# Performance work log

Hardware: AMD Instinct MI355X
Metric: run time of the kernel (lower is better)

Reference implementation:

```python
import jax, jax.numpy as jnp
import numpy as np

NUM_HEADS = 8
NUM_POINTS = 4


def _bilinear_sample(value_hw, locs, H, W):
    """grid_sample(mode='bilinear', align_corners=False, padding_mode='zeros').
    value_hw: [B, heads, H*W, hd]; locs: [B, Nq, heads, P, 2] in [0,1].
    Returns [B, Nq, heads, P, hd]."""
    B, Nq, heads, P, _ = locs.shape
    hd = value_hw.shape[-1]
    # torch maps g in [-1,1] -> pixel ((g+1)*size-1)/2; with g = 2*loc-1 this is loc*size - 0.5
    x = locs[..., 0] * W - 0.5
    y = locs[..., 1] * H - 0.5
    x0 = jnp.floor(x); y0 = jnp.floor(y)
    wx = x - x0; wy = y - y0
    ix0 = x0.astype(jnp.int32); iy0 = y0.astype(jnp.int32)
    ix1 = ix0 + 1; iy1 = iy0 + 1

    def gather(iy, ix):
        valid = (ix >= 0) & (ix < W) & (iy >= 0) & (iy < H)
        flat = jnp.clip(iy, 0, H - 1) * W + jnp.clip(ix, 0, W - 1)  # [B,Nq,heads,P]
        flat_t = flat.transpose(0, 2, 1, 3).reshape(B, heads, Nq * P)
        v = jnp.take_along_axis(value_hw, flat_t[..., None], axis=2)  # [B,heads,Nq*P,hd]
        v = v.reshape(B, heads, Nq, P, hd).transpose(0, 2, 1, 3, 4)
        return v * valid[..., None].astype(v.dtype)

    out = (gather(iy0, ix0) * ((1 - wx) * (1 - wy))[..., None]
           + gather(iy0, ix1) * (wx * (1 - wy))[..., None]
           + gather(iy1, ix0) * ((1 - wx) * wy)[..., None]
           + gather(iy1, ix1) * (wx * wy)[..., None])
    return out


def setup_inputs() -> dict:
    key = jax.random.key(0)
    ks = jax.random.split(key, 12)
    B, Nq, C, H, W = 4, 8192, 256, 128, 128
    heads, P = NUM_HEADS, NUM_POINTS
    s = 1.0 / np.sqrt(C)
    return {
        "query": jax.random.normal(ks[0], (B, Nq, C), jnp.float32),
        "reference_points": jax.random.uniform(ks[1], (B, Nq, 2), jnp.float32),
        "value": jax.random.normal(ks[2], (B, H * W, C), jnp.float32),
        "W_off": jax.random.normal(ks[3], (C, heads * P * 2), jnp.float32) * s,
        "b_off": jax.random.normal(ks[4], (heads * P * 2,), jnp.float32) * 0.5,
        "W_attn": jax.random.normal(ks[5], (C, heads * P), jnp.float32) * s,
        "b_attn": jax.random.normal(ks[6], (heads * P,), jnp.float32) * 0.1,
        "W_v": jax.random.normal(ks[7], (C, C), jnp.float32) * s,
        "b_v": jax.random.normal(ks[8], (C,), jnp.float32) * 0.1,
        "W_out": jax.random.normal(ks[9], (C, C), jnp.float32) * s,
        "b_out": jax.random.normal(ks[10], (C,), jnp.float32) * 0.1,
        "H": H,
        "W": W,
    }


def reference(query, reference_points, value, W_off, b_off, W_attn, b_attn,
              W_v, b_v, W_out, b_out, H, W):
    B, Nq, C = query.shape
    heads, P = NUM_HEADS, NUM_POINTS
    hd = C // heads

    offsets = (query @ W_off + b_off).reshape(B, Nq, heads, P, 2)
    attn = jax.nn.softmax((query @ W_attn + b_attn).reshape(B, Nq, heads, P), axis=-1)

    off_x = offsets[..., 0] / float(W) * 0.1
    off_y = offsets[..., 1] / float(H) * 0.1
    locs = reference_points[:, :, None, None, :] + jnp.stack([off_x, off_y], axis=-1)
    locs = jnp.clip(locs, 0.0, 1.0)  # [B,Nq,heads,P,2]

    # value projection -> [B, heads, H*W, hd]
    v = (value @ W_v + b_v).reshape(B, H * W, heads, hd).transpose(0, 2, 1, 3)

    sampled = _bilinear_sample(v, locs, H, W)            # [B,Nq,heads,P,hd]
    agg = jnp.einsum('bnhp,bnhpd->bnhd', attn, sampled)  # weighted sum over points
    out = agg.reshape(B, Nq, C) @ W_out + b_out
    return out
```

## Files before the change

kernel.cpp:

```cpp
#include <hip/hip_runtime.h>
#include <cstdint>

#define NB 4
#define NQ 8192
#define NC 256
#define IH 128
#define IW 128
#define NHW (IH * IW)
#define NHEADS 8
#define NP 4
#define NHD 32

typedef __bf16 bf16x8 __attribute__((ext_vector_type(8)));
typedef float f32x4 __attribute__((ext_vector_type(4)));

union FragCast { uint4 q; bf16x8 v; };

__device__ __forceinline__ unsigned int f2bf(float f) {
    unsigned int u = __float_as_uint(f);
    return (u + 0x7FFFu + ((u >> 16) & 1u)) >> 16;
}
__device__ __forceinline__ float bf2f(unsigned short s) {
    return __uint_as_float(((unsigned int)s) << 16);
}

__global__ __launch_bounds__(256) void k_pack(
    const float* __restrict__ Wv, const float* __restrict__ Wout,
    const float* __restrict__ Woff, const float* __restrict__ Wattn,
    unsigned short* __restrict__ pkv, unsigned short* __restrict__ pko,
    unsigned short* __restrict__ pkq)
{
    const int tid = blockIdx.x * 256 + threadIdx.x;
    if (tid < 4096) {
        const float* src = (tid & 2048) ? Wout : Wv;
        unsigned short* dst = (tid & 2048) ? pko : pkv;
        const int rem = tid & 2047;
        const int kt = rem >> 8, col = rem & 255;
        unsigned short* d = dst + (size_t)kt * 8192 + (col >> 4) * 512 + (col & 15) * 8;
        const float* s = src + (size_t)kt * 32 * 256 + col;
#pragma unroll
        for (int j = 0; j < 32; ++j)
            d[(j >> 3) * 128 + (j & 7)] = (unsigned short)f2bf(s[(size_t)j * 256]);
    } else {
        const int rem = tid - 4096;
        const int kt = rem / 96, col = rem % 96;
        unsigned short* d = pkq + (size_t)kt * 3072 + (col >> 4) * 512 + (col & 15) * 8;
        const float* s; int stride;
        if (col < 64) { s = Woff + col; stride = 64; }
        else          { s = Wattn + (col - 64); stride = 32; }
        s += (size_t)kt * 32 * stride;
#pragma unroll
        for (int j = 0; j < 32; ++j)
            d[(j >> 3) * 128 + (j & 7)] = (unsigned short)f2bf(s[(size_t)j * stride]);
    }
}

#define VP_TPB 4
__global__ __launch_bounds__(512) void k_vproj(
    const float* __restrict__ value, const unsigned short* __restrict__ Bpk,
    const float* __restrict__ bv, unsigned short* __restrict__ vproj)
{
    const int t = threadIdx.x;
    const int l = t & 63, w = t >> 6;
    const int mh = w & 1, cg = w >> 1;

    __shared__ unsigned short A[2][64 * 256];

    uint4 bq[8][4];
#pragma unroll
    for (int kt = 0; kt < 8; ++kt)
#pragma unroll
        for (int i = 0; i < 4; ++i)
            bq[kt][i] = *reinterpret_cast<const uint4*>(
                Bpk + (size_t)kt * 8192 + (size_t)(cg * 4 + i) * 512 + l * 8);

    float bb[4];
#pragma unroll
    for (int i = 0; i < 4; ++i) bb[i] = bv[cg * 64 + i * 16 + (l & 15)];

    const size_t tile0 = (size_t)blockIdx.x * VP_TPB;

    float4 st[8];
#pragma unroll
    for (int i = 0; i < 8; ++i) {
        const int chunk = i * 512 + t;
        const int row = chunk >> 6, k0 = (chunk & 63) * 4;
        st[i] = *reinterpret_cast<const float4*>(&value[(tile0 * 64 + row) * NC + k0]);
    }
#pragma unroll
    for (int i = 0; i < 8; ++i) {
        const int chunk = i * 512 + t;
        const int row = chunk >> 6, k0 = (chunk & 63) * 4;
        unsigned int byte = (unsigned int)(row * 512 + k0 * 2) ^ (unsigned int)((row & 7) << 4);
        *reinterpret_cast<uint2*>(reinterpret_cast<char*>(A[0]) + byte) =
            make_uint2(f2bf(st[i].x) | (f2bf(st[i].y) << 16),
                       f2bf(st[i].z) | (f2bf(st[i].w) << 16));
    }
    __syncthreads();

    for (int tt = 0; tt < VP_TPB; ++tt) {
        const int cur = tt & 1;
        if (tt + 1 < VP_TPB) {
#pragma unroll
            for (int i = 0; i < 8; ++i) {
                const int chunk = i * 512 + t;
                const int row = chunk >> 6, k0 = (chunk & 63) * 4;
                st[i] = *reinterpret_cast<const float4*>(
                    &value[((tile0 + tt + 1) * 64 + row) * NC + k0]);
            }
        }

        f32x4 acc[2][4];
#pragma unroll
        for (int m = 0; m < 2; ++m)
#pragma unroll
            for (int i = 0; i < 4; ++i) acc[m][i] = (f32x4)(bb[i]);

#pragma unroll
        for (int kt = 0; kt < 8; ++kt) {
#pragma unroll
            for (int m = 0; m < 2; ++m) {
                const int arow = mh * 32 + m * 16 + (l & 15);
                unsigned int abyte = (unsigned int)(arow * 512 + (kt * 32 + (l >> 4) * 8) * 2)
                                   ^ (unsigned int)((arow & 7) << 4);
                FragCast af;
                af.q = *reinterpret_cast<const uint4*>(reinterpret_cast<const char*>(A[cur]) + abyte);
#pragma unroll
                for (int i = 0; i < 4; ++i) {
                    FragCast bfc; bfc.q = bq[kt][i];
                    acc[m][i] = __builtin_amdgcn_mfma_f32_16x16x32_bf16(af.v, bfc.v, acc[m][i], 0, 0, 0);
                }
            }
        }

        const size_t rowbase = (tile0 + tt) * 64;
#pragma unroll
        for (int m = 0; m < 2; ++m)
#pragma unroll
            for (int i = 0; i < 4; ++i) {
                const int col = cg * 64 + i * 16 + (l & 15);
#pragma unroll
                for (int j = 0; j < 4; ++j) {
                    const size_t row = rowbase + mh * 32 + m * 16 + (l >> 4) * 4 + j;
                    vproj[row * NC + col] = (unsigned short)f2bf(acc[m][i][j]);
                }
            }

        if (tt + 1 < VP_TPB) {
#pragma unroll
            for (int i = 0; i < 8; ++i) {
                const int chunk = i * 512 + t;
                const int row = chunk >> 6, k0 = (chunk & 63) * 4;
                unsigned int byte = (unsigned int)(row * 512 + k0 * 2) ^ (unsigned int)((row & 7) << 4);
                *reinterpret_cast<uint2*>(reinterpret_cast<char*>(A[cur ^ 1]) + byte) =
                    make_uint2(f2bf(st[i].x) | (f2bf(st[i].y) << 16),
                               f2bf(st[i].z) | (f2bf(st[i].w) << 16));
            }
            __syncthreads();
        }
    }
}

__global__ __launch_bounds__(512) void k_fused(
    const float* __restrict__ query, const float* __restrict__ refp,
    const unsigned short* __restrict__ Bq, const float* __restrict__ boff,
    const float* __restrict__ battn, const unsigned short* __restrict__ vproj,
    const unsigned short* __restrict__ Bo, const float* __restrict__ bout,
    float* __restrict__ out)
{
    const int t = threadIdx.x;
    const int l = t & 63, w = t >> 6;
    const int x = blockIdx.x & 7, kk = blockIdx.x >> 3;
    const int b = x >> 1;
    const int j = (kk << 1) | (x & 1);
    const size_t q0 = (size_t)b * NQ + (size_t)j * 16;

    __shared__ unsigned short A[16 * 256];
    __shared__ float locs_s[16][64];
    __shared__ float attn_s[16][32];
    __shared__ float refs[16][2];

#pragma unroll
    for (int i = 0; i < 2; ++i) {
        const int chunk = i * 512 + t;
        const int row = chunk >> 6, k0 = (chunk & 63) * 4;
        const float4 v4 = *reinterpret_cast<const float4*>(&query[(q0 + row) * NC + k0]);
        unsigned int byte = (unsigned int)(row * 512 + k0 * 2) ^ (unsigned int)((row & 7) << 4);
        *reinterpret_cast<uint2*>(reinterpret_cast<char*>(A) + byte) =
            make_uint2(f2bf(v4.x) | (f2bf(v4.y) << 16),
                       f2bf(v4.z) | (f2bf(v4.w) << 16));
    }
    if (t < 32) reinterpret_cast<float*>(refs)[t] = refp[q0 * 2 + t];
    __syncthreads();

    if (w < 6) {
        const int arow = l & 15, achunk = l >> 4;
        f32x4 acc = (f32x4)(0.f);
#pragma unroll
        for (int kt = 0; kt < 8; ++kt) {
            unsigned int abyte = (unsigned int)(arow * 512 + (kt * 32 + achunk * 8) * 2)
                               ^ (unsigned int)((arow & 7) << 4);
            FragCast af;
            af.q = *reinterpret_cast<const uint4*>(reinterpret_cast<const char*>(A) + abyte);
            FragCast bfc;
            bfc.q = *reinterpret_cast<const uint4*>(Bq + (size_t)kt * 3072 + w * 512 + l * 8);
            acc = __builtin_amdgcn_mfma_f32_16x16x32_bf16(af.v, bfc.v, acc, 0, 0, 0);
        }
        const int col = w * 16 + arow;
        if (col < 64) {
            const float bias = boff[col];
            const int xy = col & 1;
#pragma unroll
            for (int jj = 0; jj < 4; ++jj) {
                const int row = achunk * 4 + jj;
                float off = acc[jj] + bias;
                float loc = refs[row][xy] + off * (0.1f / 128.0f);
                locs_s[row][col] = fminf(fmaxf(loc, 0.f), 1.f);
            }
        } else {
            const int lc = col - 64;
            const float bias = battn[lc];
#pragma unroll
            for (int jj = 0; jj < 4; ++jj) {
                const int row = achunk * 4 + jj;
                float v = acc[jj] + bias;
                float m = fmaxf(v, __shfl_xor(v, 1));
                m = fmaxf(m, __shfl_xor(m, 2));
                float e = __expf(v - m);
                float s = e + __shfl_xor(e, 1);
                s = s + __shfl_xor(s, 2);
                attn_s[row][lc] = e / s;
            }
        }
    }
    __syncthreads();

    {
        const int q = t >> 5, h = (t >> 2) & 7, c = t & 3;
        const char* __restrict__ vb =
            reinterpret_cast<const char*>(vproj) + (size_t)b * NHW * 512;
        const unsigned int laneoff = (unsigned int)(h * 64 + c * 16);

        float wts[16];
        unsigned int offs[16];
#pragma unroll
        for (int p = 0; p < 4; ++p) {
            const float lx = locs_s[q][h * 8 + p * 2 + 0];
            const float ly = locs_s[q][h * 8 + p * 2 + 1];
            const float aw = attn_s[q][h * 4 + p];
            const float xx = lx * (float)IW - 0.5f;
            const float yy = ly * (float)IH - 0.5f;
            const float x0f = floorf(xx), y0f = floorf(yy);
            const float wx = xx - x0f, wy = yy - y0f;
            const int ix0 = (int)x0f, iy0 = (int)y0f;
            const int ix1 = ix0 + 1, iy1 = iy0 + 1;
            const int cx0 = max(ix0, 0), cy0 = max(iy0, 0);
            const int cx1 = min(ix1, IW - 1), cy1 = min(iy1, IH - 1);
            const float vx0 = (ix0 >= 0) ? 1.f : 0.f;
            const float vy0 = (iy0 >= 0) ? 1.f : 0.f;
            const float vx1 = (ix1 < IW) ? 1.f : 0.f;
            const float vy1 = (iy1 < IH) ? 1.f : 0.f;
            wts[p * 4 + 0] = aw * ((1.f - wx) * (1.f - wy) * vx0 * vy0);
            wts[p * 4 + 1] = aw * (wx * (1.f - wy) * vx1 * vy0);
            wts[p * 4 + 2] = aw * ((1.f - wx) * wy * vx0 * vy1);
            wts[p * 4 + 3] = aw * (wx * wy * vx1 * vy1);
            offs[p * 4 + 0] = (unsigned int)(cy0 * IW + cx0) * 512u + laneoff;
            offs[p * 4 + 1] = (unsigned int)(cy0 * IW + cx1) * 512u + laneoff;
            offs[p * 4 + 2] = (unsigned int)(cy1 * IW + cx0) * 512u + laneoff;
            offs[p * 4 + 3] = (unsigned int)(cy1 * IW + cx1) * 512u + laneoff;
        }

        uint4 vals[16];
#pragma unroll
        for (int jj = 0; jj < 16; ++jj)
            vals[jj] = *reinterpret_cast<const uint4*>(vb + offs[jj]);

        float acc[8];
#pragma unroll
        for (int e = 0; e < 8; ++e) acc[e] = 0.f;
#pragma unroll
        for (int jj = 0; jj < 16; ++jj) {
            const unsigned short* u = reinterpret_cast<const unsigned short*>(&vals[jj]);
            const float wj = wts[jj];
#pragma unroll
            for (int e = 0; e < 8; ++e) acc[e] = fmaf(wj, bf2f(u[e]), acc[e]);
        }

        uint4 pk;
        pk.x = f2bf(acc[0]) | (f2bf(acc[1]) << 16);
        pk.y = f2bf(acc[2]) | (f2bf(acc[3]) << 16);
        pk.z = f2bf(acc[4]) | (f2bf(acc[5]) << 16);
        pk.w = f2bf(acc[6]) | (f2bf(acc[7]) << 16);
        unsigned int byte = (unsigned int)(q * 512 + (h * NHD + c * 8) * 2)
                          ^ (unsigned int)((q & 7) << 4);
        *reinterpret_cast<uint4*>(reinterpret_cast<char*>(A) + byte) = pk;
    }
    __syncthreads();

    {
        const int arow = l & 15, achunk = l >> 4;
        f32x4 acc2[2];
#pragma unroll
        for (int i = 0; i < 2; ++i) acc2[i] = (f32x4)(0.f);

#pragma unroll
        for (int kt = 0; kt < 8; ++kt) {
            unsigned int abyte = (unsigned int)(arow * 512 + (kt * 32 + achunk * 8) * 2)
                               ^ (unsigned int)((arow & 7) << 4);
            FragCast af;
            af.q = *reinterpret_cast<const uint4*>(reinterpret_cast<const char*>(A) + abyte);
#pragma unroll
            for (int i = 0; i < 2; ++i) {
                const int ct = w * 2 + i;
                FragCast bfc;
                bfc.q = *reinterpret_cast<const uint4*>(Bo + (size_t)kt * 8192 + ct * 512 + l * 8);
                acc2[i] = __builtin_amdgcn_mfma_f32_16x16x32_bf16(af.v, bfc.v, acc2[i], 0, 0, 0);
            }
        }

#pragma unroll
        for (int i = 0; i < 2; ++i) {
            const int col = (w * 2 + i) * 16 + arow;
            const float bbv = bout[col];
#pragma unroll
            for (int jj = 0; jj < 4; ++jj) {
                const size_t row = q0 + achunk * 4 + jj;
                out[row * NC + col] = acc2[i][jj] + bbv;
            }
        }
    }
}

extern "C" void kernel_launch(void* const* d_in, const int* in_sizes, int n_in,
                              void* d_out, int out_size, void* d_ws, size_t ws_size,
                              hipStream_t stream) {
    const float* query = (const float*)d_in[0];
    const float* refp  = (const float*)d_in[1];
    const float* value = (const float*)d_in[2];
    const float* Woff  = (const float*)d_in[3];
    const float* boff  = (const float*)d_in[4];
    const float* Wattn = (const float*)d_in[5];
    const float* battn = (const float*)d_in[6];
    const float* Wv    = (const float*)d_in[7];
    const float* bv    = (const float*)d_in[8];
    const float* Wout  = (const float*)d_in[9];
    const float* bout  = (const float*)d_in[10];
    float* out = (float*)d_out;

    unsigned short* vproj  = (unsigned short*)d_ws;
    unsigned short* WvPk   = vproj + (size_t)NB * NHW * NC;
    unsigned short* WoutPk = WvPk + (size_t)NC * NC;
    unsigned short* WqPk   = WoutPk + (size_t)NC * NC;

    k_pack<<<dim3(19), dim3(256), 0, stream>>>(Wv, Wout, Woff, Wattn, WvPk, WoutPk, WqPk);
    k_vproj<<<dim3(256), dim3(512), 0, stream>>>(value, WvPk, bv, vproj);
    k_fused<<<dim3(NB * NQ / 16), dim3(512), 0, stream>>>(query, refp, WqPk, boff, battn,
                                                          vproj, WoutPk, bout, out);
}
```

Baseline: 67.33 us.

## Sort queries by spatial bin of reference point for gather locality

Adds a counting sort (count, scan, scatter kernels) that groups queries into 16x16 spatial bins by reference point, then has the fused kernel process queries in that order using an indirection array. The goal is to make each block's bilinear gathers from the projected value tensor hit nearby pixels, which improves cache reuse. In exchange it adds four small launches, including a memset and a single-thread serial scan, and replaces contiguous query loads and output stores with indirect row accesses. Atomic-based slot assignment makes the order within a bin nondeterministic, but the output is unaffected.

Result: slower. 83.56 us (+24.1%).

```diff
diff --git a/kernel.cpp b/kernel.cpp
--- a/kernel.cpp
+++ b/kernel.cpp
@@ -22,6 +22,43 @@
 }
 __device__ __forceinline__ float bf2f(unsigned short s) {
     return __uint_as_float(((unsigned int)s) << 16);
+}
+__device__ __forceinline__ int ref_bin(float rx, float ry) {
+    int bx = (int)(rx * 16.0f); bx = bx > 15 ? 15 : (bx < 0 ? 0 : bx);
+    int by = (int)(ry * 16.0f); by = by > 15 ? 15 : (by < 0 ? 0 : by);
+    return by * 16 + bx;
+}
+
+__global__ __launch_bounds__(256) void k_count(
+    const float* __restrict__ refp, int* __restrict__ cnt)
+{
+    const int tid = blockIdx.x * 256 + threadIdx.x;
+    const int b = tid >> 13;
+    const int bin = ref_bin(refp[(size_t)tid * 2], refp[(size_t)tid * 2 + 1]);
+    atomicAdd(&cnt[b * 256 + bin], 1);
+}
+
+__global__ __launch_bounds__(64) void k_scan(
+    const int* __restrict__ cnt, int* __restrict__ pos)
+{
+    const int b = threadIdx.x;
+    if (b < NB) {
+        int run = b * NQ;
+        for (int i = 0; i < 256; ++i) {
+            pos[b * 256 + i] = run;
+            run += cnt[b * 256 + i];
+        }
+    }
+}
+
+__global__ __launch_bounds__(256) void k_scatter(
+    const float* __restrict__ refp, int* __restrict__ pos, int* __restrict__ order)
+{
+    const int tid = blockIdx.x * 256 + threadIdx.x;
+    const int b = tid >> 13;
+    const int bin = ref_bin(refp[(size_t)tid * 2], refp[(size_t)tid * 2 + 1]);
+    const int slot = atomicAdd(&pos[b * 256 + bin], 1);
+    order[slot] = tid & (NQ - 1);
 }
 
 __global__ __launch_bounds__(256) void k_pack(
@@ -166,31 +203,39 @@
     const unsigned short* __restrict__ Bq, const float* __restrict__ boff,
     const float* __restrict__ battn, const unsigned short* __restrict__ vproj,
     const unsigned short* __restrict__ Bo, const float* __restrict__ bout,
-    float* __restrict__ out)
+    const int* __restrict__ order, float* __restrict__ out)
 {
     const int t = threadIdx.x;
     const int l = t & 63, w = t >> 6;
     const int x = blockIdx.x & 7, kk = blockIdx.x >> 3;
     const int b = x >> 1;
     const int j = (kk << 1) | (x & 1);
-    const size_t q0 = (size_t)b * NQ + (size_t)j * 16;
 
     __shared__ unsigned short A[16 * 256];
     __shared__ float locs_s[16][64];
     __shared__ float attn_s[16][32];
     __shared__ float refs[16][2];
+    __shared__ int ord_s[16];
+
+    if (t < 16) ord_s[t] = order[(size_t)b * NQ + j * 16 + t];
+    __syncthreads();
 
 #pragma unroll
     for (int i = 0; i < 2; ++i) {
         const int chunk = i * 512 + t;
         const int row = chunk >> 6, k0 = (chunk & 63) * 4;
-        const float4 v4 = *reinterpret_cast<const float4*>(&query[(q0 + row) * NC + k0]);
+        const size_t grow = (size_t)b * NQ + ord_s[row];
+        const float4 v4 = *reinterpret_cast<const float4*>(&query[grow * NC + k0]);
         unsigned int byte = (unsigned int)(row * 512 + k0 * 2) ^ (unsigned int)((row & 7) << 4);
         *reinterpret_cast<uint2*>(reinterpret_cast<char*>(A) + byte) =
             make_uint2(f2bf(v4.x) | (f2bf(v4.y) << 16),
                        f2bf(v4.z) | (f2bf(v4.w) << 16));
     }
-    if (t < 32) reinterpret_cast<float*>(refs)[t] = refp[q0 * 2 + t];
+    if (t < 32) {
+        const int r = t >> 1;
+        const size_t grow = (size_t)b * NQ + ord_s[r];
+        refs[r][t & 1] = refp[grow * 2 + (t & 1)];
+    }
     __syncthreads();
 
     if (w < 6) {
@@ -324,7 +369,7 @@
             const float bbv = bout[col];
 #pragma unroll
             for (int jj = 0; jj < 4; ++jj) {
-                const size_t row = q0 + achunk * 4 + jj;
+                const size_t row = (size_t)b * NQ + ord_s[achunk * 4 + jj];
                 out[row * NC + col] = acc2[i][jj] + bbv;
             }
         }
@@ -351,9 +396,16 @@
     unsigned short* WvPk   = vproj + (size_t)NB * NHW * NC;
     unsigned short* WoutPk = WvPk + (size_t)NC * NC;
     unsigned short* WqPk   = WoutPk + (size_t)NC * NC;
-
+    int* cnt   = (int*)(WqPk + (size_t)NC * 96);
+    int* pos   = cnt + NB * 256;
+    int* order = pos + NB * 256;
+
+    hipMemsetAsync(cnt, 0, NB * 256 * sizeof(int), stream);
+    k_count<<<dim3(NB * NQ / 256), dim3(256), 0, stream>>>(refp, cnt);
+    k_scan<<<dim3(1), dim3(64), 0, stream>>>(cnt, pos);
+    k_scatter<<<dim3(NB * NQ / 256), dim3(256), 0, stream>>>(refp, pos, order);
     k_pack<<<dim3(19), dim3(256), 0, stream>>>(Wv, Wout, Woff, Wattn, WvPk, WoutPk, WqPk);
     k_vproj<<<dim3(256), dim3(512), 0, stream>>>(value, WvPk, bv, vproj);
     k_fused<<<dim3(NB * NQ / 16), dim3(512), 0, stream>>>(query, refp, WqPk, boff, battn,
-                                                          vproj, WoutPk, bout, out);
-}
+                                                          vproj, WoutPk, bout, order, out);
+}
```
